# Optimization experiments

Hardware: AMD Instinct MI355X
Metric: run time of the kernel (lower is better)

## Reference

```python
import jax, jax.numpy as jnp
import numpy as np

N_NODES = 100000
N_EDGES = 1600000
IN_DIM = 256
OUT_DIM = 128
BATCH = 8192
SLOPE = 0.1
EPS = 1e-8


def setup_inputs() -> dict:
    key = jax.random.key(0)
    k1, k2, k3, k4, k5, k6, k7 = jax.random.split(key, 7)
    feats = jax.random.normal(k1, (N_NODES, IN_DIM), dtype=jnp.float32)
    W = jax.random.normal(k2, (IN_DIM, OUT_DIM), dtype=jnp.float32) / np.sqrt(IN_DIM)
    b = jax.random.normal(k3, (OUT_DIM,), dtype=jnp.float32) * 0.01
    a = jax.random.normal(k4, (2 * OUT_DIM,), dtype=jnp.float32) / np.sqrt(2 * OUT_DIM)
    r = jax.random.randint(k5, (N_EDGES,), 0, N_NODES, dtype=jnp.int64)
    c = jax.random.randint(k6, (N_EDGES,), 0, N_NODES, dtype=jnp.int64)
    batch_idx = jax.random.randint(k7, (BATCH,), 0, N_NODES, dtype=jnp.int64)
    return {"feats": feats, "W": W, "b": b, "a": a, "r": r, "c": c, "batch_idx": batch_idx}


def reference(feats, W, b, a, r, c, batch_idx):
    d = W.shape[1]
    new_emb = feats @ W + b                      # [N, d]
    # [h_r || h_c] @ a  ==  h_r @ a[:d] + h_c @ a[d:]
    s_src = new_emb @ a[:d]                      # [N]
    s_dst = new_emb @ a[d:]                      # [N]
    e = jnp.exp(jax.nn.leaky_relu(s_src[r] + s_dst[c], negative_slope=SLOPE))  # [E]
    denom = jax.ops.segment_sum(e, r, num_segments=N_NODES)                    # [N]
    num = jax.ops.segment_sum(e[:, None] * new_emb[c], r, num_segments=N_NODES)  # [N, d]
    out = num / (denom[:, None] + EPS)
    return out[batch_idx]
```

## Files before the change

### kernel.cpp

```cpp
#include <hip/hip_runtime.h>

#define N_NODES 100000
#define N_EDGES 1600000
#define IN_DIM  256
#define OUT_DIM 128
#define BATCH_N 8192
#define SLOPE   0.1f
#define EPS_V   1e-8f
#define BUCKET_CAP 96

__global__ __launch_bounds__(256) void prep_kernel(const float* __restrict__ W,
                                                   const float* __restrict__ b,
                                                   const float* __restrict__ a,
                                                   float* __restrict__ uv,
                                                   float* __restrict__ consts) {
  int t = threadIdx.x;
  float su = 0.f, sv = 0.f;
  for (int j = 0; j < OUT_DIM; j++) {
    float w = W[t * OUT_DIM + j];
    su += w * a[j];
    sv += w * a[OUT_DIM + j];
  }
  uv[t] = su;
  uv[IN_DIM + t] = sv;

  __shared__ float red[256];
  float pb = (t < OUT_DIM) ? b[t] : 0.f;
  red[t] = (t < OUT_DIM) ? pb * a[t] : 0.f;
  __syncthreads();
  for (int off = 128; off > 0; off >>= 1) {
    if (t < off) red[t] += red[t + off];
    __syncthreads();
  }
  if (t == 0) consts[0] = red[0];
  __syncthreads();
  red[t] = (t < OUT_DIM) ? pb * a[OUT_DIM + t] : 0.f;
  __syncthreads();
  for (int off = 128; off > 0; off >>= 1) {
    if (t < off) red[t] += red[t + off];
    __syncthreads();
  }
  if (t == 0) consts[1] = red[0];
}

__global__ __launch_bounds__(256) void init_kernel(int* __restrict__ slot, int* __restrict__ cursor) {
  int i = blockIdx.x * blockDim.x + threadIdx.x;
  if (i < N_NODES) slot[i] = -1;
  if (i < BATCH_N) cursor[i] = 0;
}

__global__ __launch_bounds__(256) void slots_kernel(const int* __restrict__ batch_idx, int* __restrict__ slot) {
  int i = blockIdx.x * blockDim.x + threadIdx.x;
  if (i < BATCH_N) slot[batch_idx[i]] = i;
}

__global__ __launch_bounds__(256) void scores_kernel(const float* __restrict__ feats,
                                                     const float* __restrict__ uv,
                                                     const float* __restrict__ consts,
                                                     float* __restrict__ s_src,
                                                     float* __restrict__ s_dst) {
  int wid = (blockIdx.x * blockDim.x + threadIdx.x) >> 6;
  int lane = threadIdx.x & 63;
  if (wid >= N_NODES) return;
  float4 f  = *(const float4*)&feats[(size_t)wid * IN_DIM + lane * 4];
  float4 u4 = *(const float4*)&uv[lane * 4];
  float4 v4 = *(const float4*)&uv[IN_DIM + lane * 4];
  float p1 = f.x * u4.x + f.y * u4.y + f.z * u4.z + f.w * u4.w;
  float p2 = f.x * v4.x + f.y * v4.y + f.z * v4.z + f.w * v4.w;
#pragma unroll
  for (int s = 32; s > 0; s >>= 1) {
    p1 += __shfl_xor(p1, s);
    p2 += __shfl_xor(p2, s);
  }
  if (lane == 0) {
    s_src[wid] = p1 + consts[0];
    s_dst[wid] = p2 + consts[1];
  }
}

__global__ __launch_bounds__(256) void scatter_kernel(const int* __restrict__ r, const int* __restrict__ c,
                                                      const int* __restrict__ slot,
                                                      const float* __restrict__ s_src,
                                                      const float* __restrict__ s_dst,
                                                      int* __restrict__ cursor,
                                                      int* __restrict__ bucket_c, float* __restrict__ bucket_e) {
  int i = blockIdx.x * blockDim.x + threadIdx.x;
  if (i >= N_EDGES) return;
  int rr = r[i];
  int sl = slot[rr];
  if (sl < 0) return;
  int cc = c[i];
  float x = s_src[rr] + s_dst[cc];
  float lr = x > 0.f ? x : SLOPE * x;
  float e = expf(lr);
  int pos = atomicAdd(&cursor[sl], 1);
  if (pos < BUCKET_CAP) {
    bucket_c[sl * BUCKET_CAP + pos] = cc;
    bucket_e[sl * BUCKET_CAP + pos] = e;
  }
}

__global__ __launch_bounds__(256) void agg_kernel(const float* __restrict__ feats,
                                                  const int* __restrict__ cursor,
                                                  const int* __restrict__ bucket_c,
                                                  const float* __restrict__ bucket_e,
                                                  float* __restrict__ aggw,
                                                  float* __restrict__ scale_b) {
  int wid = (blockIdx.x * blockDim.x + threadIdx.x) >> 6;
  int lane = threadIdx.x & 63;
  if (wid >= BATCH_N) return;
  int cnt = cursor[wid];
  cnt = cnt > BUCKET_CAP ? BUCKET_CAP : cnt;
  int base = wid * BUCKET_CAP;
  float ax = 0.f, ay = 0.f, az = 0.f, aw = 0.f, den = 0.f;
#pragma unroll 2
  for (int j = 0; j < cnt; j++) {
    int cc  = bucket_c[base + j];
    float e = bucket_e[base + j];
    float4 f = *(const float4*)&feats[(size_t)cc * IN_DIM + lane * 4];
    ax += e * f.x; ay += e * f.y; az += e * f.z; aw += e * f.w;
    den += e;
  }
  float dinv = 1.f / (den + EPS_V);
  *(float4*)&aggw[(size_t)wid * IN_DIM + lane * 4] =
      make_float4(ax * dinv, ay * dinv, az * dinv, aw * dinv);
  if (lane == 0) scale_b[wid] = den * dinv;
}

__global__ __launch_bounds__(256) void gemm2_kernel(const float* __restrict__ aggw,
                                                    const float* __restrict__ W,
                                                    const float* __restrict__ b,
                                                    const float* __restrict__ scale_b,
                                                    float* __restrict__ out) {
  __shared__ float As[32][33];
  __shared__ float Ws[32][128];
  const int t = threadIdx.x;
  const int row0 = blockIdx.x * 32;
  const int tx = t & 31;
  const int ty = t >> 5;

  float acc[4][4];
#pragma unroll
  for (int i = 0; i < 4; i++)
#pragma unroll
    for (int j = 0; j < 4; j++) acc[i][j] = 0.f;

  for (int k0 = 0; k0 < IN_DIM; k0 += 32) {
    {
      int row = t >> 3, c4 = t & 7;
      float4 v = *(const float4*)&aggw[(size_t)(row0 + row) * IN_DIM + k0 + c4 * 4];
      As[c4 * 4 + 0][row] = v.x;
      As[c4 * 4 + 1][row] = v.y;
      As[c4 * 4 + 2][row] = v.z;
      As[c4 * 4 + 3][row] = v.w;
    }
#pragma unroll
    for (int p = 0; p < 4; p++) {
      int id = t + p * 256;
      int kr = id >> 5, c4 = id & 31;
      *(float4*)&Ws[kr][c4 * 4] = *(const float4*)&W[(size_t)(k0 + kr) * OUT_DIM + c4 * 4];
    }
    __syncthreads();
#pragma unroll
    for (int k = 0; k < 32; k++) {
      float av[4];
#pragma unroll
      for (int i = 0; i < 4; i++) av[i] = As[k][ty * 4 + i];
      float4 w4 = *(const float4*)&Ws[k][tx * 4];
#pragma unroll
      for (int i = 0; i < 4; i++) {
        acc[i][0] += av[i] * w4.x; acc[i][1] += av[i] * w4.y;
        acc[i][2] += av[i] * w4.z; acc[i][3] += av[i] * w4.w;
      }
    }
    __syncthreads();
  }
  float4 b4 = *(const float4*)&b[tx * 4];
#pragma unroll
  for (int i = 0; i < 4; i++) {
    int row = row0 + ty * 4 + i;
    float sb = scale_b[row];
    *(float4*)&out[(size_t)row * OUT_DIM + tx * 4] =
        make_float4(acc[i][0] + sb * b4.x, acc[i][1] + sb * b4.y,
                    acc[i][2] + sb * b4.z, acc[i][3] + sb * b4.w);
  }
}

__global__ __launch_bounds__(256) void fix_kernel(const int* __restrict__ batch_idx,
                                                  const int* __restrict__ slot,
                                                  float* __restrict__ out) {
  int wid = (blockIdx.x * blockDim.x + threadIdx.x) >> 6;
  int lane = threadIdx.x & 63;
  if (wid >= BATCH_N) return;
  int sl = slot[batch_idx[wid]];
  if (sl == wid) return;
  float2 v = *(const float2*)&out[(size_t)sl * OUT_DIM + lane * 2];
  *(float2*)&out[(size_t)wid * OUT_DIM + lane * 2] = v;
}

extern "C" void kernel_launch(void* const* d_in, const int* in_sizes, int n_in,
                              void* d_out, int out_size, void* d_ws, size_t ws_size,
                              hipStream_t stream) {
  const float* feats     = (const float*)d_in[0];
  const float* W         = (const float*)d_in[1];
  const float* b         = (const float*)d_in[2];
  const float* a         = (const float*)d_in[3];
  const int*   r         = (const int*)d_in[4];
  const int*   c         = (const int*)d_in[5];
  const int*   batch_idx = (const int*)d_in[6];
  float* out = (float*)d_out;

  float* uv       = (float*)d_ws;
  float* consts   = uv + 2 * IN_DIM;
  float* s_src    = consts + 8;
  float* s_dst    = s_src + N_NODES;
  int*   slot     = (int*)(s_dst + N_NODES);
  int*   cursor   = slot + N_NODES;
  float* scale_b  = (float*)(cursor + BATCH_N);
  int*   bucket_c = (int*)(scale_b + BATCH_N);
  float* bucket_e = (float*)(bucket_c + (size_t)BATCH_N * BUCKET_CAP);
  float* aggw     = bucket_e + (size_t)BATCH_N * BUCKET_CAP;

  prep_kernel<<<1, 256, 0, stream>>>(W, b, a, uv, consts);
  init_kernel<<<(N_NODES + 255) / 256, 256, 0, stream>>>(slot, cursor);
  slots_kernel<<<(BATCH_N + 255) / 256, 256, 0, stream>>>(batch_idx, slot);
  scores_kernel<<<(N_NODES * 64 + 255) / 256, 256, 0, stream>>>(feats, uv, consts, s_src, s_dst);
  scatter_kernel<<<(N_EDGES + 255) / 256, 256, 0, stream>>>(r, c, slot, s_src, s_dst,
                                                            cursor, bucket_c, bucket_e);
  agg_kernel<<<(BATCH_N * 64 + 255) / 256, 256, 0, stream>>>(feats, cursor, bucket_c, bucket_e,
                                                             aggw, scale_b);
  gemm2_kernel<<<BATCH_N / 32, 256, 0, stream>>>(aggw, W, b, scale_b, out);
  fix_kernel<<<(BATCH_N * 64 + 255) / 256, 256, 0, stream>>>(batch_idx, slot, out);
}
```

Before: 246.1 us.

## Split each batch node's edge aggregation across four wavefronts with shared-memory reduction

The aggregation kernel now assigns one 256-thread block per batch slot instead of one wavefront, and the four wavefronts take interleaved edges. The bucket's column indices and edge weights are first staged into shared memory, and partial sums are combined through shared memory before normalization. This is meant to raise memory-level parallelism on the gather of feature rows (about 16 edges per node). In exchange it adds two block barriers and a reduction per node, and launches four times as many threads.

```diff
diff --git a/kernel.cpp b/kernel.cpp
--- a/kernel.cpp
+++ b/kernel.cpp
@@ -106,25 +106,45 @@
                                                   const float* __restrict__ bucket_e,
                                                   float* __restrict__ aggw,
                                                   float* __restrict__ scale_b) {
-  int wid = (blockIdx.x * blockDim.x + threadIdx.x) >> 6;
-  int lane = threadIdx.x & 63;
-  if (wid >= BATCH_N) return;
-  int cnt = cursor[wid];
+  __shared__ int   sc[BUCKET_CAP];
+  __shared__ float se[BUCKET_CAP];
+  __shared__ float red[4][256];
+  __shared__ float dred[4];
+  const int sl = blockIdx.x;
+  const int t = threadIdx.x, w = t >> 6, lane = t & 63;
+  int cnt = cursor[sl];
   cnt = cnt > BUCKET_CAP ? BUCKET_CAP : cnt;
-  int base = wid * BUCKET_CAP;
+  if (t < cnt) {
+    sc[t] = bucket_c[sl * BUCKET_CAP + t];
+    se[t] = bucket_e[sl * BUCKET_CAP + t];
+  }
+  __syncthreads();
   float ax = 0.f, ay = 0.f, az = 0.f, aw = 0.f, den = 0.f;
 #pragma unroll 2
-  for (int j = 0; j < cnt; j++) {
-    int cc  = bucket_c[base + j];
-    float e = bucket_e[base + j];
+  for (int j = w; j < cnt; j += 4) {
+    int cc  = sc[j];
+    float e = se[j];
     float4 f = *(const float4*)&feats[(size_t)cc * IN_DIM + lane * 4];
     ax += e * f.x; ay += e * f.y; az += e * f.z; aw += e * f.w;
     den += e;
   }
-  float dinv = 1.f / (den + EPS_V);
-  *(float4*)&aggw[(size_t)wid * IN_DIM + lane * 4] =
-      make_float4(ax * dinv, ay * dinv, az * dinv, aw * dinv);
-  if (lane == 0) scale_b[wid] = den * dinv;
+  *(float4*)&red[w][lane * 4] = make_float4(ax, ay, az, aw);
+  if (lane == 0) dred[w] = den;
+  __syncthreads();
+  if (w == 0) {
+    float4 r0 = *(float4*)&red[0][lane * 4];
+    float4 r1 = *(float4*)&red[1][lane * 4];
+    float4 r2 = *(float4*)&red[2][lane * 4];
+    float4 r3 = *(float4*)&red[3][lane * 4];
+    float d = dred[0] + dred[1] + dred[2] + dred[3];
+    float dinv = 1.f / (d + EPS_V);
+    *(float4*)&aggw[(size_t)sl * IN_DIM + lane * 4] =
+        make_float4((r0.x + r1.x + r2.x + r3.x) * dinv,
+                    (r0.y + r1.y + r2.y + r3.y) * dinv,
+                    (r0.z + r1.z + r2.z + r3.z) * dinv,
+                    (r0.w + r1.w + r2.w + r3.w) * dinv);
+    if (lane == 0) scale_b[sl] = d * dinv;
+  }
 }
 
 __global__ __launch_bounds__(256) void gemm2_kernel(const float* __restrict__ aggw,
@@ -227,8 +247,7 @@
   scores_kernel<<<(N_NODES * 64 + 255) / 256, 256, 0, stream>>>(feats, uv, consts, s_src, s_dst);
   scatter_kernel<<<(N_EDGES + 255) / 256, 256, 0, stream>>>(r, c, slot, s_src, s_dst,
                                                             cursor, bucket_c, bucket_e);
-  agg_kernel<<<(BATCH_N * 64 + 255) / 256, 256, 0, stream>>>(feats, cursor, bucket_c, bucket_e,
-                                                             aggw, scale_b);
+  agg_kernel<<<BATCH_N, 256, 0, stream>>>(feats, cursor, bucket_c, bucket_e, aggw, scale_b);
   gemm2_kernel<<<BATCH_N / 32, 256, 0, stream>>>(aggw, W, b, scale_b, out);
   fix_kernel<<<(BATCH_N * 64 + 255) / 256, 256, 0, stream>>>(batch_idx, slot, out);
 }
```

Result: no change. 245.1 us (-0.4%).
